# Optimization experiments

Measured on AMD Instinct MI355X. Metric: run time of the kernel, lower is better.

Reference implementation:

```python
import jax, jax.numpy as jnp
import numpy as np

N_NODES = 100000
N_EDGES = 1600000
DIM = 128
N_LAYERS = 3
BN_EPS = 1e-5


def setup_inputs() -> dict:
    key = jax.random.key(0)
    ks = jax.random.split(key, 8)
    x = jax.random.normal(ks[0], (N_NODES, DIM), dtype=jnp.float32)
    edge_index = jax.random.randint(ks[1], (2, N_EDGES), 0, N_NODES, dtype=jnp.int64)
    batch = jax.random.randint(ks[2], (N_NODES,), 0, 64, dtype=jnp.int64)
    # stacked per-layer params (input_dim == hidden_dim == 128)
    W = jax.random.normal(ks[3], (N_LAYERS, DIM, DIM), dtype=jnp.float32) / np.sqrt(DIM)
    b = jnp.zeros((N_LAYERS, DIM), dtype=jnp.float32)
    gamma = jax.random.normal(ks[4], (N_LAYERS, DIM), dtype=jnp.float32) * 0.1 + 1.0
    beta = jax.random.normal(ks[5], (N_LAYERS, DIM), dtype=jnp.float32) * 0.1
    running_mean = jax.random.normal(ks[6], (N_LAYERS, DIM), dtype=jnp.float32) * 0.1
    running_var = jax.random.uniform(ks[7], (N_LAYERS, DIM), dtype=jnp.float32, minval=0.5, maxval=1.5)
    return {"x": x, "edge_index": edge_index, "batch": batch, "W": W, "b": b,
            "gamma": gamma, "beta": beta,
            "running_mean": running_mean, "running_var": running_var}


def reference(x, edge_index, batch, W, b, gamma, beta, running_mean, running_var):
    # batch is unused by the original forward (kept for signature fidelity)
    n = x.shape[0]
    # GCNConv adds self-loops once per layer; precompute augmented edge list + norm
    loops = jnp.arange(n, dtype=edge_index.dtype)
    src = jnp.concatenate([edge_index[0], loops])
    dst = jnp.concatenate([edge_index[1], loops])
    deg = jax.ops.segment_sum(jnp.ones_like(dst, dtype=x.dtype), dst, num_segments=n)
    dinv = jax.lax.rsqrt(jnp.maximum(deg, 1e-12))
    norm = dinv[src] * dinv[dst]  # [E+N]

    h = x
    for l in range(N_LAYERS):
        # GCNConv: propagate normalized messages of (h @ W), then add bias
        hw = h @ W[l]                                   # [N, D]
        msg = hw[src] * norm[:, None]                   # gather  [E+N, D]
        h = jax.ops.segment_sum(msg, dst, num_segments=n) + b[l]
        # BatchNorm1d (eval mode: running stats) + ReLU; dropout is identity in eval
        h = gamma[l] * (h - running_mean[l]) * jax.lax.rsqrt(running_var[l] + BN_EPS) + beta[l]
        h = jax.nn.relu(h)
    return h
```

## Files before the change

### kernel.cpp

```cpp
#include <hip/hip_runtime.h>

#define N_NODES 100000
#define N_EDGES 1600000
#define DIM 128
#define BN_EPS 1e-5f
#define BM 64
#define BSHIFT 9
#define BN 512
#define NB 196
#define CAP 10240
#define CHUNK 4096

typedef _Float16 f16;
typedef _Float16 f16x2 __attribute__((ext_vector_type(2)));
typedef _Float16 f16x4 __attribute__((ext_vector_type(4)));
typedef _Float16 f16x8 __attribute__((ext_vector_type(8)));
typedef float f32x4 __attribute__((ext_vector_type(4)));


__global__ void k_bzero(int* __restrict__ bcnt) {
  int t = threadIdx.x;
  if (t < NB) bcnt[t] = 0;
}

__global__ __launch_bounds__(256) void k_binA(const int* __restrict__ src,
                                              const int* __restrict__ dst,
                                              int* __restrict__ bcnt,
                                              int2* __restrict__ stage) {
  __shared__ int hist[NB];
  __shared__ int lofs[NB];
  __shared__ int lbase[NB];
  __shared__ int lcur[NB];
  __shared__ int scanbuf[256];
  __shared__ int2 buf[CHUNK];
  int t = threadIdx.x;
  for (int i = t; i < NB; i += 256) { hist[i] = 0; lcur[i] = 0; }
  __syncthreads();
  int e0 = blockIdx.x * CHUNK;
  int en = min(CHUNK, N_EDGES - e0);
  for (int i = t; i < en; i += 256) {
    unsigned d = (unsigned)dst[e0 + i];
    unsigned s = (unsigned)src[e0 + i];
    if (d < N_NODES && s < N_NODES) atomicAdd(&hist[d >> BSHIFT], 1);
  }
  __syncthreads();
  scanbuf[t] = (t < NB) ? hist[t] : 0;
  __syncthreads();
  for (int off = 1; off < 256; off <<= 1) {
    int x = (t >= off) ? scanbuf[t - off] : 0;
    __syncthreads();
    scanbuf[t] += x;
    __syncthreads();
  }
  if (t < NB) {
    lofs[t] = scanbuf[t] - hist[t];
    lbase[t] = atomicAdd(&bcnt[t], hist[t]);
  }
  __syncthreads();
  for (int i = t; i < en; i += 256) {
    int d = dst[e0 + i], s = src[e0 + i];
    if ((unsigned)d < N_NODES && (unsigned)s < N_NODES) {
      int b = d >> BSHIFT;
      int r = atomicAdd(&lcur[b], 1);
      buf[lofs[b] + r] = make_int2(d, s);
    }
  }
  __syncthreads();
  int tot = lofs[NB - 1] + hist[NB - 1];
  for (int i = t; i < tot; i += 256) {
    int2 p = buf[i];
    int b = p.x >> BSHIFT;
    int goff = lbase[b] + (i - lofs[b]);
    if (goff < CAP) stage[(size_t)b * CAP + goff] = p;
  }
}

__global__ __launch_bounds__(256) void k_bscan(const int* __restrict__ bcnt,
                                               int* __restrict__ bbase) {
  __shared__ int sb[256];
  int t = threadIdx.x;
  int v = (t < NB) ? min(bcnt[t], CAP) : 0;
  sb[t] = v;
  __syncthreads();
  for (int off = 1; off < 256; off <<= 1) {
    int x = (t >= off) ? sb[t - off] : 0;
    __syncthreads();
    sb[t] += x;
    __syncthreads();
  }
  if (t < NB) bbase[t] = sb[t] - v;
}

__global__ __launch_bounds__(512) void k_binB(const int2* __restrict__ stage,
                                              const int* __restrict__ bcnt,
                                              const int* __restrict__ bbase,
                                              int* __restrict__ rowptr,
                                              int* __restrict__ col,
                                              float* __restrict__ dinv) {
  __shared__ int cnt[BN];
  __shared__ int offs[BN];
  __shared__ int lcur[BN];
  __shared__ int sb[BN];
  __shared__ int colbuf[CAP];
  int b = blockIdx.x, t = threadIdx.x;
  int base = b << BSHIFT;
  int nn = min(BN, N_NODES - base);
  int m = min(bcnt[b], CAP);
  const int2* seg = stage + (size_t)b * CAP;
  cnt[t] = 0; lcur[t] = 0;
  __syncthreads();
  for (int i = t; i < m; i += 512) atomicAdd(&cnt[seg[i].x - base], 1);
  __syncthreads();
  sb[t] = cnt[t];
  __syncthreads();
  for (int off = 1; off < 512; off <<= 1) {
    int x = (t >= off) ? sb[t - off] : 0;
    __syncthreads();
    sb[t] += x;
    __syncthreads();
  }
  offs[t] = sb[t] - cnt[t];
  __syncthreads();
  for (int i = t; i < m; i += 512) {
    int2 p = seg[i];
    int dl = p.x - base;
    int r = atomicAdd(&lcur[dl], 1);
    colbuf[offs[dl] + r] = p.y;
  }
  __syncthreads();
  int gb = bbase[b];
  if (t < nn) {
    rowptr[base + t] = gb + offs[t];
    dinv[base + t] = rsqrtf((float)(cnt[t] + 1));
  }
  if (b == NB - 1 && t == 0) rowptr[N_NODES] = gb + m;
  for (int i = t; i < m; i += 512) col[gb + i] = colbuf[i];
}


__global__ void k_x16(const float* __restrict__ x, f16* __restrict__ h16) {
  int i = blockIdx.x * blockDim.x + threadIdx.x;
  if (i < N_NODES * DIM / 4) {
    float4 v = ((const float4*)x)[i];
    f16x4 o = {(f16)v.x, (f16)v.y, (f16)v.z, (f16)v.w};
    ((f16x4*)h16)[i] = o;
  }
}

__global__ void k_wprep(const float* __restrict__ W, f16* __restrict__ Wt) {
  int t = blockIdx.x * blockDim.x + threadIdx.x;
  if (t < DIM * DIM) {
    int c = t >> 7, k = t & 127;
    Wt[t] = (f16)W[k * DIM + c];
  }
}

__global__ void k_bnprep(const float* __restrict__ b, const float* __restrict__ gamma,
                         const float* __restrict__ beta, const float* __restrict__ mean,
                         const float* __restrict__ var, float* __restrict__ scsh) {
  int t = threadIdx.x;
  if (t < 384) {
    int l = t >> 7, c = t & 127, i = l * DIM + c;
    float sc = gamma[i] * rsqrtf(var[i] + BN_EPS);
    scsh[l * 256 + c] = sc;
    scsh[l * 256 + 128 + c] = sc * (b[i] - mean[i]) + beta[i];
  }
}


__global__ __launch_bounds__(256) void k_gemm16(const f16* __restrict__ H16,
                                                const f16* __restrict__ Wt16,
                                                const float* __restrict__ dinv,
                                                f16* __restrict__ HWS16) {
  __shared__ f16x8 Hs[BM * 16];
  __shared__ f16x8 WtS[DIM * 16];
  int t = threadIdx.x;
  int row0 = blockIdx.x * BM;

  const f16x8* Hg = (const f16x8*)H16;
  #pragma unroll
  for (int i = 0; i < 4; i++) {
    int q = t + i * 256;
    int r = q >> 4, s = q & 15;
    int gr = row0 + r; if (gr >= N_NODES) gr = N_NODES - 1;
    Hs[r * 16 + (s ^ (r & 7))] = Hg[(size_t)gr * 16 + s];
  }
  const f16x8* Wg = (const f16x8*)Wt16;
  #pragma unroll
  for (int i = 0; i < 8; i++) {
    int q = t + i * 256;
    int c = q >> 4, s = q & 15;
    WtS[c * 16 + (s ^ (c & 7))] = Wg[(size_t)c * 16 + s];
  }
  __syncthreads();

  int wid = t >> 6, l = t & 63;
  int wrow = wid * 16;
  int lr = l & 15, lg = l >> 4;

  int r = wrow + lr, rx = r & 7, rbase = r * 16;
  f16x8 afr[4];
  #pragma unroll
  for (int kk = 0; kk < 4; kk++) afr[kk] = Hs[rbase + ((kk * 4 + lg) ^ rx)];

  f32x4 acc[8] = {};
  #pragma unroll
  for (int ct = 0; ct < 8; ct++) {
    int c = ct * 16 + lr, cx = c & 7, cbase = c * 16;
    #pragma unroll
    for (int kk = 0; kk < 4; kk++) {
      f16x8 bfr = WtS[cbase + ((kk * 4 + lg) ^ cx)];
      acc[ct] = __builtin_amdgcn_mfma_f32_16x16x32_f16(afr[kk], bfr, acc[ct], 0, 0, 0);
    }
  }

  int orow = row0 + wrow + lg * 4;
  #pragma unroll
  for (int i = 0; i < 4; i++) {
    int gr = orow + i;
    if (gr < N_NODES) {
      float dv = dinv[gr];
      #pragma unroll
      for (int ct = 0; ct < 8; ct++)
        HWS16[(size_t)gr * DIM + ct * 16 + lr] = (f16)(acc[ct][i] * dv);
    }
  }
}


__global__ __launch_bounds__(256) void k_gather1(const f16* __restrict__ HWS,
                                                 const int* __restrict__ rowptr,
                                                 const int* __restrict__ col,
                                                 const float* __restrict__ dinv,
                                                 const float* __restrict__ scsh,
                                                 float* __restrict__ outF,
                                                 f16* __restrict__ outH,
                                                 int last) {
  int gw = (int)((blockIdx.x * blockDim.x + threadIdx.x) >> 6);
  int lane = threadIdx.x & 63;
  int eg = lane >> 4;
  int cs = lane & 15;
  int wid = gw * 4 + eg;
  if (wid >= N_NODES) return;
  int beg = rowptr[wid];
  int cnt = rowptr[wid + 1] - beg + 1;
  const f16x8* h8 = (const f16x8*)HWS;

  f16x8 a0 = {}, a1 = {}, a2 = {}, a3 = {};
  int j = 0;
  for (; j + 3 < cnt; j += 4) {
    int s0 = (j == 0) ? wid : col[beg + j - 1];
    int s1 = col[beg + j];
    int s2 = col[beg + j + 1];
    int s3 = col[beg + j + 2];
    a0 += h8[(size_t)s0 * 16 + cs];
    a1 += h8[(size_t)s1 * 16 + cs];
    a2 += h8[(size_t)s2 * 16 + cs];
    a3 += h8[(size_t)s3 * 16 + cs];
  }
  for (; j < cnt; j++) {
    int s0 = (j == 0) ? wid : col[beg + j - 1];
    a0 += h8[(size_t)s0 * 16 + cs];
  }
  a0 += a1; a2 += a3; a0 += a2;

  float di = dinv[wid];
  int c4 = cs * 2;
  const f32x4* scv = (const f32x4*)scsh;
  const f32x4* shv = (const f32x4*)(scsh + 128);
  float o[8];
  #pragma unroll
  for (int half = 0; half < 2; half++) {
    f32x4 sc = scv[c4 + half], sh = shv[c4 + half];
    #pragma unroll
    for (int i = 0; i < 4; i++) {
      float v = (float)a0[half * 4 + i] * di;
      o[half * 4 + i] = fmaxf(fmaf(v, sc[i], sh[i]), 0.f);
    }
  }
  if (last) {
    f32x4* of = (f32x4*)outF;
    f32x4 lo = {o[0], o[1], o[2], o[3]}, hi = {o[4], o[5], o[6], o[7]};
    of[(size_t)wid * 32 + c4] = lo;
    of[(size_t)wid * 32 + c4 + 1] = hi;
  } else {
    f16x8 oh = {(f16)o[0], (f16)o[1], (f16)o[2], (f16)o[3],
                (f16)o[4], (f16)o[5], (f16)o[6], (f16)o[7]};
    ((f16x8*)outH)[(size_t)wid * 16 + cs] = oh;
  }
}


extern "C" void kernel_launch(void* const* d_in, const int* in_sizes, int n_in,
                              void* d_out, int out_size, void* d_ws, size_t ws_size,
                              hipStream_t stream) {
  const float* x = (const float*)d_in[0];
  const int* ei = (const int*)d_in[1];
  const int* srcv = ei;
  const int* dstv = ei + N_EDGES;
  const float* W     = (const float*)d_in[3];
  const float* b     = (const float*)d_in[4];
  const float* gamma = (const float*)d_in[5];
  const float* beta  = (const float*)d_in[6];
  const float* rmean = (const float*)d_in[7];
  const float* rvar  = (const float*)d_in[8];
  float* out = (float*)d_out;

  const size_t off_rowptr = 0;
  const size_t off_col    = 400128;
  const size_t off_dinv   = 6800128;
  const size_t off_bcnt   = 7200128;
  const size_t off_bbase  = 7201024;
  const size_t off_scsh   = 7201920;
  const size_t off_wt     = 7205248;
  const size_t off_h16    = 7238016;
  const size_t off_hws    = 7238016 + 25600000;
  const size_t need = off_hws + (size_t)N_NODES * DIM * sizeof(f16);
  if (ws_size < need) return;

  char* ws = (char*)d_ws;
  int*   rowptr = (int*)(ws + off_rowptr);
  int*   col    = (int*)(ws + off_col);
  float* dinv   = (float*)(ws + off_dinv);
  int*   bcnt   = (int*)(ws + off_bcnt);
  int*   bbase  = (int*)(ws + off_bbase);
  float* scsh   = (float*)(ws + off_scsh);
  f16*   wt16   = (f16*)(ws + off_wt);
  f16*   h16    = (f16*)(ws + off_h16);
  int2*  stage  = (int2*)(ws + off_h16);
  f16*   hws16  = (f16*)(ws + off_hws);

  k_bzero<<<1, 256, 0, stream>>>(bcnt);
  k_binA<<<(N_EDGES + CHUNK - 1) / CHUNK, 256, 0, stream>>>(srcv, dstv, bcnt, stage);
  k_bscan<<<1, 256, 0, stream>>>(bcnt, bbase);
  k_binB<<<NB, 512, 0, stream>>>(stage, bcnt, bbase, rowptr, col, dinv);
  k_x16<<<12500, 256, 0, stream>>>(x, h16);
  k_bnprep<<<1, 384, 0, stream>>>(b, gamma, beta, rmean, rvar, scsh);

  for (int l = 0; l < 3; l++) {
    k_wprep<<<64, 256, 0, stream>>>(W + l * DIM * DIM, wt16);
    k_gemm16<<<(N_NODES + BM - 1) / BM, 256, 0, stream>>>(h16, wt16, dinv, hws16);
    k_gather1<<<6250, 256, 0, stream>>>(hws16, rowptr, col, dinv, scsh + l * 256,
                                        out, h16, (l == 2) ? 1 : 0);
  }
}
```

Measured before the change: 299.8 us.

## Pad CSR rows to multiples of four with per-bucket fixed slots and packed rowptr

Replaces the global prefix-scanned CSR with per-bucket fixed-capacity column slots, removing the k_bscan kernel. Each row is padded to a multiple of four with a dummy index pointing at a zeroed extra row. Offset and degree are packed into one int, so dinv is recomputed from the degree rather than loaded. The gather kernel loads column indices as int4 and issues eight gathers per iteration without a self-loop branch. The risks are extra padded gather traffic, and silent edge drops if a bucket overflows its capacity or a per-bucket offset exceeds the 14-bit packing limit.

After: 283.5 us. 1.06x faster.

```diff
diff --git a/kernel.cpp b/kernel.cpp
--- a/kernel.cpp
+++ b/kernel.cpp
@@ -8,11 +8,11 @@
 #define BSHIFT 9
 #define BN 512
 #define NB 196
-#define CAP 10240
+#define CAP_S 9216
+#define CAP_C 10048
 #define CHUNK 4096
 
 typedef _Float16 f16;
-typedef _Float16 f16x2 __attribute__((ext_vector_type(2)));
 typedef _Float16 f16x4 __attribute__((ext_vector_type(4)));
 typedef _Float16 f16x8 __attribute__((ext_vector_type(8)));
 typedef float f32x4 __attribute__((ext_vector_type(4)));
@@ -71,47 +71,31 @@
     int2 p = buf[i];
     int b = p.x >> BSHIFT;
     int goff = lbase[b] + (i - lofs[b]);
-    if (goff < CAP) stage[(size_t)b * CAP + goff] = p;
-  }
-}
-
-__global__ __launch_bounds__(256) void k_bscan(const int* __restrict__ bcnt,
-                                               int* __restrict__ bbase) {
-  __shared__ int sb[256];
-  int t = threadIdx.x;
-  int v = (t < NB) ? min(bcnt[t], CAP) : 0;
-  sb[t] = v;
-  __syncthreads();
-  for (int off = 1; off < 256; off <<= 1) {
-    int x = (t >= off) ? sb[t - off] : 0;
-    __syncthreads();
-    sb[t] += x;
-    __syncthreads();
-  }
-  if (t < NB) bbase[t] = sb[t] - v;
+    if (goff < CAP_S) stage[(size_t)b * CAP_S + goff] = p;
+  }
 }
 
 __global__ __launch_bounds__(512) void k_binB(const int2* __restrict__ stage,
                                               const int* __restrict__ bcnt,
-                                              const int* __restrict__ bbase,
-                                              int* __restrict__ rowptr,
-                                              int* __restrict__ col,
-                                              float* __restrict__ dinv) {
+                                              int* __restrict__ rowpack,
+                                              int* __restrict__ col) {
   __shared__ int cnt[BN];
   __shared__ int offs[BN];
   __shared__ int lcur[BN];
   __shared__ int sb[BN];
-  __shared__ int colbuf[CAP];
+  __shared__ int mp_s;
+  __shared__ int colbuf[CAP_C];
   int b = blockIdx.x, t = threadIdx.x;
   int base = b << BSHIFT;
   int nn = min(BN, N_NODES - base);
-  int m = min(bcnt[b], CAP);
-  const int2* seg = stage + (size_t)b * CAP;
+  int m = min(bcnt[b], CAP_S);
+  const int2* seg = stage + (size_t)b * CAP_S;
   cnt[t] = 0; lcur[t] = 0;
   __syncthreads();
   for (int i = t; i < m; i += 512) atomicAdd(&cnt[seg[i].x - base], 1);
   __syncthreads();
-  sb[t] = cnt[t];
+  int pcnt = (cnt[t] + 3) & ~3;
+  sb[t] = pcnt;
   __syncthreads();
   for (int off = 1; off < 512; off <<= 1) {
     int x = (t >= off) ? sb[t - off] : 0;
@@ -119,22 +103,30 @@
     sb[t] += x;
     __syncthreads();
   }
-  offs[t] = sb[t] - cnt[t];
+  offs[t] = sb[t] - pcnt;
+  if (t == 511) mp_s = sb[511];
   __syncthreads();
   for (int i = t; i < m; i += 512) {
     int2 p = seg[i];
     int dl = p.x - base;
     int r = atomicAdd(&lcur[dl], 1);
-    colbuf[offs[dl] + r] = p.y;
-  }
-  __syncthreads();
-  int gb = bbase[b];
+    int o = offs[dl] + r;
+    if (o < CAP_C) colbuf[o] = p.y;
+  }
+  __syncthreads();
+  {
+    int o = offs[t], c = cnt[t], pc = (c + 3) & ~3;
+    for (int k = c; k < pc; k++)
+      if (o + k < CAP_C) colbuf[o + k] = N_NODES;
+  }
+  __syncthreads();
   if (t < nn) {
-    rowptr[base + t] = gb + offs[t];
-    dinv[base + t] = rsqrtf((float)(cnt[t] + 1));
-  }
-  if (b == NB - 1 && t == 0) rowptr[N_NODES] = gb + m;
-  for (int i = t; i < m; i += 512) col[gb + i] = colbuf[i];
+    int o = offs[t], c = cnt[t];
+    if (o + ((c + 3) & ~3) > CAP_C) { o = 0; c = 0; }
+    rowpack[base + t] = (o << 14) | c;
+  }
+  int mp = min(mp_s, CAP_C);
+  for (int i = t; i < mp; i += 512) col[b * CAP_C + i] = colbuf[i];
 }
 
 
@@ -147,11 +139,16 @@
   }
 }
 
-__global__ void k_wprep(const float* __restrict__ W, f16* __restrict__ Wt) {
+__global__ void k_wprep(const float* __restrict__ W, f16* __restrict__ Wt,
+                        f16* __restrict__ hws) {
   int t = blockIdx.x * blockDim.x + threadIdx.x;
   if (t < DIM * DIM) {
     int c = t >> 7, k = t & 127;
     Wt[t] = (f16)W[k * DIM + c];
+  }
+  if (blockIdx.x == 0 && threadIdx.x < 16) {
+    f16x8 z = {};
+    ((f16x8*)(hws + (size_t)N_NODES * DIM))[threadIdx.x] = z;
   }
 }
 
@@ -170,7 +167,7 @@
 
 __global__ __launch_bounds__(256) void k_gemm16(const f16* __restrict__ H16,
                                                 const f16* __restrict__ Wt16,
-                                                const float* __restrict__ dinv,
+                                                const int* __restrict__ rowpack,
                                                 f16* __restrict__ HWS16) {
   __shared__ f16x8 Hs[BM * 16];
   __shared__ f16x8 WtS[DIM * 16];
@@ -219,7 +216,7 @@
   for (int i = 0; i < 4; i++) {
     int gr = orow + i;
     if (gr < N_NODES) {
-      float dv = dinv[gr];
+      float dv = rsqrtf((float)(rowpack[gr] & 0x3FFF) + 1.0f);
       #pragma unroll
       for (int ct = 0; ct < 8; ct++)
         HWS16[(size_t)gr * DIM + ct * 16 + lr] = (f16)(acc[ct][i] * dv);
@@ -228,43 +225,52 @@
 }
 
 
-__global__ __launch_bounds__(256) void k_gather1(const f16* __restrict__ HWS,
-                                                 const int* __restrict__ rowptr,
+__global__ __launch_bounds__(256) void k_gather8(const f16* __restrict__ HWS,
+                                                 const int* __restrict__ rowpack,
                                                  const int* __restrict__ col,
-                                                 const float* __restrict__ dinv,
                                                  const float* __restrict__ scsh,
                                                  float* __restrict__ outF,
                                                  f16* __restrict__ outH,
                                                  int last) {
-  int gw = (int)((blockIdx.x * blockDim.x + threadIdx.x) >> 6);
-  int lane = threadIdx.x & 63;
-  int eg = lane >> 4;
-  int cs = lane & 15;
-  int wid = gw * 4 + eg;
+  int tid = blockIdx.x * 256 + threadIdx.x;
+  int wid = tid >> 4;
+  int cs = tid & 15;
   if (wid >= N_NODES) return;
-  int beg = rowptr[wid];
-  int cnt = rowptr[wid + 1] - beg + 1;
+  int rp = rowpack[wid];
+  int deg = rp & 0x3FFF;
+  int off = rp >> 14;
+  int pdeg = (deg + 3) & ~3;
+  int beg = (wid >> BSHIFT) * CAP_C + off;
   const f16x8* h8 = (const f16x8*)HWS;
 
-  f16x8 a0 = {}, a1 = {}, a2 = {}, a3 = {};
+  f16x8 a0 = h8[(size_t)wid * 16 + cs];
+  f16x8 a1 = {}, a2 = {}, a3 = {};
   int j = 0;
-  for (; j + 3 < cnt; j += 4) {
-    int s0 = (j == 0) ? wid : col[beg + j - 1];
-    int s1 = col[beg + j];
-    int s2 = col[beg + j + 1];
-    int s3 = col[beg + j + 2];
-    a0 += h8[(size_t)s0 * 16 + cs];
-    a1 += h8[(size_t)s1 * 16 + cs];
-    a2 += h8[(size_t)s2 * 16 + cs];
-    a3 += h8[(size_t)s3 * 16 + cs];
-  }
-  for (; j < cnt; j++) {
-    int s0 = (j == 0) ? wid : col[beg + j - 1];
-    a0 += h8[(size_t)s0 * 16 + cs];
+  for (; j + 8 <= pdeg; j += 8) {
+    int4 c0 = *(const int4*)(col + beg + j);
+    int4 c1 = *(const int4*)(col + beg + j + 4);
+    f16x8 v0 = h8[(size_t)c0.x * 16 + cs];
+    f16x8 v1 = h8[(size_t)c0.y * 16 + cs];
+    f16x8 v2 = h8[(size_t)c0.z * 16 + cs];
+    f16x8 v3 = h8[(size_t)c0.w * 16 + cs];
+    f16x8 v4 = h8[(size_t)c1.x * 16 + cs];
+    f16x8 v5 = h8[(size_t)c1.y * 16 + cs];
+    f16x8 v6 = h8[(size_t)c1.z * 16 + cs];
+    f16x8 v7 = h8[(size_t)c1.w * 16 + cs];
+    a0 += v0; a1 += v1; a2 += v2; a3 += v3;
+    a0 += v4; a1 += v5; a2 += v6; a3 += v7;
+  }
+  if (j < pdeg) {
+    int4 c0 = *(const int4*)(col + beg + j);
+    f16x8 v0 = h8[(size_t)c0.x * 16 + cs];
+    f16x8 v1 = h8[(size_t)c0.y * 16 + cs];
+    f16x8 v2 = h8[(size_t)c0.z * 16 + cs];
+    f16x8 v3 = h8[(size_t)c0.w * 16 + cs];
+    a0 += v0; a1 += v1; a2 += v2; a3 += v3;
   }
   a0 += a1; a2 += a3; a0 += a2;
 
-  float di = dinv[wid];
+  float di = rsqrtf((float)(deg + 1));
   int c4 = cs * 2;
   const f32x4* scv = (const f32x4*)scsh;
   const f32x4* shv = (const f32x4*)(scsh + 128);
@@ -306,41 +312,35 @@
   const float* rvar  = (const float*)d_in[8];
   float* out = (float*)d_out;
 
-  const size_t off_rowptr = 0;
-  const size_t off_col    = 400128;
-  const size_t off_dinv   = 6800128;
-  const size_t off_bcnt   = 7200128;
-  const size_t off_bbase  = 7201024;
-  const size_t off_scsh   = 7201920;
-  const size_t off_wt     = 7205248;
-  const size_t off_h16    = 7238016;
-  const size_t off_hws    = 7238016 + 25600000;
-  const size_t need = off_hws + (size_t)N_NODES * DIM * sizeof(f16);
+  const size_t off_rowpack = 0;
+  const size_t off_col     = 400128;
+  const size_t off_scsh    = 400128 + 7877632;
+  const size_t off_wt      = off_scsh + 3072;
+  const size_t off_h16     = off_wt + 32768;
+  const size_t off_hws     = off_h16 + 25600000;
+  const size_t need = off_hws + (size_t)(N_NODES + 1) * DIM * sizeof(f16);
   if (ws_size < need) return;
 
   char* ws = (char*)d_ws;
-  int*   rowptr = (int*)(ws + off_rowptr);
-  int*   col    = (int*)(ws + off_col);
-  float* dinv   = (float*)(ws + off_dinv);
-  int*   bcnt   = (int*)(ws + off_bcnt);
-  int*   bbase  = (int*)(ws + off_bbase);
-  float* scsh   = (float*)(ws + off_scsh);
-  f16*   wt16   = (f16*)(ws + off_wt);
-  f16*   h16    = (f16*)(ws + off_h16);
-  int2*  stage  = (int2*)(ws + off_h16);
-  f16*   hws16  = (f16*)(ws + off_hws);
+  int*   rowpack = (int*)(ws + off_rowpack);
+  int*   col     = (int*)(ws + off_col);
+  float* scsh    = (float*)(ws + off_scsh);
+  f16*   wt16    = (f16*)(ws + off_wt);
+  f16*   h16     = (f16*)(ws + off_h16);
+  int2*  stage   = (int2*)(ws + off_h16);
+  f16*   hws16   = (f16*)(ws + off_hws);
+  int*   bcnt    = (int*)(ws + off_hws);
 
   k_bzero<<<1, 256, 0, stream>>>(bcnt);
   k_binA<<<(N_EDGES + CHUNK - 1) / CHUNK, 256, 0, stream>>>(srcv, dstv, bcnt, stage);
-  k_bscan<<<1, 256, 0, stream>>>(bcnt, bbase);
-  k_binB<<<NB, 512, 0, stream>>>(stage, bcnt, bbase, rowptr, col, dinv);
+  k_binB<<<NB, 512, 0, stream>>>(stage, bcnt, rowpack, col);
   k_x16<<<12500, 256, 0, stream>>>(x, h16);
   k_bnprep<<<1, 384, 0, stream>>>(b, gamma, beta, rmean, rvar, scsh);
 
   for (int l = 0; l < 3; l++) {
-    k_wprep<<<64, 256, 0, stream>>>(W + l * DIM * DIM, wt16);
-    k_gemm16<<<(N_NODES + BM - 1) / BM, 256, 0, stream>>>(h16, wt16, dinv, hws16);
-    k_gather1<<<6250, 256, 0, stream>>>(hws16, rowptr, col, dinv, scsh + l * 256,
+    k_wprep<<<64, 256, 0, stream>>>(W + l * DIM * DIM, wt16, hws16);
+    k_gemm16<<<(N_NODES + BM - 1) / BM, 256, 0, stream>>>(h16, wt16, rowpack, hws16);
+    k_gather8<<<6250, 256, 0, stream>>>(hws16, rowpack, col, scsh + l * 256,
                                         out, h16, (l == 2) ? 1 : 0);
   }
 }
```
